# Optimization experiments

Measured on AMD Instinct MI355X. Metric: run time of the kernel, lower is better.

The kernel has to match this reference:

```python
import jax, jax.numpy as jnp
import numpy as np

N = 4096
FIN = 4096
LOC = 16
H1, H2, HEADS = 120, 50, 4
H1_PER = H1 // HEADS
FILM_Z = 32
SSDB_H = 60
N_HEMI = N // 2
NEG_SLOPE = 0.1
GATE_BIAS = -2.0
MASK_FILL = -9e15


def leaky(x):
    return jax.nn.leaky_relu(x, negative_slope=NEG_SLOPE)


def gat(x, mask, W, a_src, a_dst, bias, concat):
    # x: (N, Fin), W: (H, Fin, O), a_src/a_dst: (H, O), mask: (N, N) bool
    wh = jnp.einsum('nf,hfo->hno', x, W)            # (H, N, O)
    f1 = jnp.einsum('hno,ho->hn', wh, a_src)        # (H, N)
    f2 = jnp.einsum('hno,ho->hn', wh, a_dst)        # (H, N)
    e = leaky(f1[:, :, None] + f2[:, None, :])      # (H, N, N)
    e = jnp.where(mask[None], e, MASK_FILL)
    alpha = jax.nn.softmax(e, axis=-1)
    out = jnp.einsum('hij,hjo->hio', alpha, wh)     # (H, N, O)
    if concat:
        h, n, o = out.shape
        out2 = out.transpose(1, 0, 2).reshape(n, h * o)
    else:
        out2 = out.mean(axis=0)
    return out2 + bias


def _uni(k, shape, stdv):
    return jax.random.uniform(k, shape, jnp.float32, -stdv, stdv)


def setup_inputs() -> dict:
    key = jax.random.key(0)
    ks = jax.random.split(key, 30)
    s1 = 1.0 / np.sqrt(H1_PER)
    s2 = 1.0 / np.sqrt(H2)
    inp = {
        'x_fc': jax.random.normal(ks[0], (N, FIN), jnp.float32),
        'adj': jax.random.randint(ks[1], (N, N), 0, 2, jnp.int32),
        'l_loc': jax.random.uniform(ks[2], (N, LOC), jnp.float32),
        # gat1
        'W1': _uni(ks[3], (HEADS, FIN, H1_PER), s1),
        'a1s': _uni(ks[4], (HEADS, H1_PER), s1),
        'a1d': _uni(ks[5], (HEADS, H1_PER), s1),
        'b1': _uni(ks[6], (H1,), s1),
        # gat2
        'W2': _uni(ks[7], (1, H1, H2), s2),
        'a2s': _uni(ks[8], (1, H2), s2),
        'a2d': _uni(ks[9], (1, H2), s2),
        'b2': _uni(ks[10], (H2,), s2),
        # classifier (no bias)
        'Wc': _uni(ks[11], (2, H2), s2),
        # FiLM trunk
        'Wl1': _uni(ks[12], (FILM_Z, LOC), 1.0 / np.sqrt(LOC)),
        'bl1': _uni(ks[13], (FILM_Z,), 1.0 / np.sqrt(LOC)),
        'Wl2': _uni(ks[14], (FILM_Z, FILM_Z), 1.0 / np.sqrt(FILM_Z)),
        'bl2': _uni(ks[15], (FILM_Z,), 1.0 / np.sqrt(FILM_Z)),
        'Wg': _uni(ks[16], (H2, FILM_Z), 1.0 / np.sqrt(FILM_Z)),
        'bg': _uni(ks[17], (H2,), 1.0 / np.sqrt(FILM_Z)),
        'Wb': _uni(ks[18], (H2, FILM_Z), 1.0 / np.sqrt(FILM_Z)),
        'bb': _uni(ks[19], (H2,), 1.0 / np.sqrt(FILM_Z)),
        'Wgate': _uni(ks[20], (1, FILM_Z), 1.0 / np.sqrt(FILM_Z)),
        'bgate': jnp.full((1,), GATE_BIAS, jnp.float32),
        # SSDB hemi
        'Ws1': _uni(ks[21], (SSDB_H, N_HEMI), 1.0 / np.sqrt(N_HEMI)),
        'bs1': _uni(ks[22], (SSDB_H,), 1.0 / np.sqrt(N_HEMI)),
        'Ws2': _uni(ks[23], (1, SSDB_H), 1.0 / np.sqrt(SSDB_H)),
        'bs2': _uni(ks[24], (1,), 1.0 / np.sqrt(SSDB_H)),
    }
    return inp


def reference(x_fc, adj, l_loc, W1, a1s, a1d, b1, W2, a2s, a2d, b2, Wc,
              Wl1, bl1, Wl2, bl2, Wg, bg, Wb, bb, Wgate, bgate,
              Ws1, bs1, Ws2, bs2):
    mask = adj > 0
    h = leaky(gat(x_fc, mask, W1, a1s, a1d, b1, concat=True))    # (N, 120)
    h = leaky(gat(h, mask, W2, a2s, a2d, b2, concat=False))      # (N, 50)
    # FiLM conditioning
    z = leaky(l_loc @ Wl1.T + bl1)
    z = leaky(z @ Wl2.T + bl2)
    gamma = z @ Wg.T + bg                                        # (N, 50)
    beta = z @ Wb.T + bb                                         # (N, 50)
    g = jax.nn.sigmoid(z @ Wgate.T + bgate)                      # (N, 1)
    cov = jnp.clip(l_loc[:, -1], 0.0, 1.0)                       # coverage_power = 1.0
    g = g * cov[:, None]
    h_fused = h + g * (gamma * h + beta)
    logits = leaky(h_fused @ Wc.T)                               # (N, 2)
    # hemisphere SSDB bias
    t = logits.T                                                 # (2, N)
    ipsi = t[:, :N_HEMI]
    contra = t[:, N_HEMI:2 * N_HEMI]
    h_i = leaky(ipsi @ Ws1.T + bs1)                              # (2, 60)
    h_c = leaky(contra @ Ws1.T + bs1)
    b_i = leaky(h_i @ Ws2.T + bs2)                               # (2, 1)
    b_c = leaky(h_c @ Ws2.T + bs2)
    b_mid = 0.5 * (b_i + b_c)                                    # (2, 1)
    bias_nodes = jnp.concatenate([
        jnp.broadcast_to(b_i.T, (N_HEMI, 2)),
        jnp.broadcast_to(b_c.T, (N_HEMI, 2)),
    ], axis=0)                                                   # n_mid = 0
    logits = logits + bias_nodes
    bias_avg = b_mid[:, 0]                                       # (2,)
    return logits, bias_avg
```

## Files before the change

kernel.cpp:

```cpp
#include <hip/hip_runtime.h>

#define NN 4096
#define NNP 4128
#define BROW 132
#define HEADS 4
#define H1PER 30
#define H1DIM 120
#define H2DIM 50

typedef short short8_t __attribute__((ext_vector_type(8)));
typedef float f32x4 __attribute__((ext_vector_type(4)));

__device__ __forceinline__ float lrelu(float x) { return x > 0.f ? x : 0.1f * x; }

__device__ __forceinline__ unsigned short bfrne(float x) {
  unsigned u = __float_as_uint(x);
  u += 0x7fffu + ((u >> 16) & 1u);
  return (unsigned short)(u >> 16);
}
__device__ __forceinline__ unsigned bfpk_rne(float lo, float hi) {
  return (unsigned)bfrne(lo) | ((unsigned)bfrne(hi) << 16);
}
__device__ __forceinline__ unsigned bfpk(float lo, float hi) {
  unsigned a = (__float_as_uint(lo) + 0x8000u) >> 16;
  unsigned b = (__float_as_uint(hi) + 0x8000u) & 0xffff0000u;
  return a | b;
}
__device__ __forceinline__ unsigned fenc(float x) {
  unsigned u = __float_as_uint(x);
  return (u & 0x80000000u) ? ~u : (u | 0x80000000u);
}
__device__ __forceinline__ float fdec(unsigned u) {
  return (u & 0x80000000u) ? __uint_as_float(u ^ 0x80000000u) : __uint_as_float(~u);
}

#define GL16(g, l)                                                                        \
  __builtin_amdgcn_global_load_lds((const __attribute__((address_space(1))) unsigned int*)(g), \
                                   (__attribute__((address_space(3))) unsigned int*)(l), 16, 0, 0)

__global__ __launch_bounds__(256) void k_bits(const int* __restrict__ adj,
                                              unsigned long long* __restrict__ bits,
                                              const float* __restrict__ W1,
                                              const float* __restrict__ a1s,
                                              const float* __restrict__ a1d,
                                              unsigned short* __restrict__ w1t,
                                              unsigned* __restrict__ mxu) {
  int t = threadIdx.x;
  if (blockIdx.x >= 16384) {
    if (blockIdx.x == 16384 && t < 8) mxu[t] = 0;
    int k = (blockIdx.x - 16384) * 256 + t;
#pragma unroll
    for (int h = 0; h < 4; ++h) {
      const float* wp = W1 + ((size_t)h * 4096 + k) * H1PER;
      float fs = 0.f, fd = 0.f;
#pragma unroll
      for (int oo = 0; oo < H1PER; ++oo) {
        float v = wp[oo];
        w1t[(size_t)(h * 30 + oo) * NNP + k] = bfrne(v);
        fs += v * a1s[h * H1PER + oo];
        fd += v * a1d[h * H1PER + oo];
      }
      w1t[(size_t)(120 + h) * NNP + k] = bfrne(fs);
      w1t[(size_t)(124 + h) * NNP + k] = bfrne(fd);
    }
    return;
  }
  int n = blockIdx.x >> 2, r = blockIdx.x & 3;
  size_t base = (size_t)n * 4096 + r * 1024;
  int v0 = adj[base + t];
  int v1 = adj[base + 256 + t];
  int v2 = adj[base + 512 + t];
  int v3 = adj[base + 768 + t];
  unsigned long long m0 = __ballot(v0 > 0);
  unsigned long long m1 = __ballot(v1 > 0);
  unsigned long long m2 = __ballot(v2 > 0);
  unsigned long long m3 = __ballot(v3 > 0);
  if ((t & 63) == 0) {
    size_t w = (size_t)n * (BROW / 2) + r * 16 + (t >> 6);
    bits[w] = m0;
    bits[w + 4] = m1;
    bits[w + 8] = m2;
    bits[w + 12] = m3;
  }
}

__global__ __launch_bounds__(256) void k_gemm1s(const float* __restrict__ x,
                                                const unsigned short* __restrict__ w1t,
                                                float* __restrict__ part) {
  const int t = threadIdx.x;
  const int lane = t & 63, wave = t >> 6;
  const int m = lane & 15, q = lane >> 4;
  const int i0 = blockIdx.x * 128;
  const int kz = blockIdx.y * 512;
  __shared__ float xs[128 * 64];
  __shared__ unsigned short bs[128 * 64];
  const int ar_ = t >> 4, ac_ = t & 15;
  const float* gxa = x + (size_t)(i0 + ar_) * 4096 + kz + (ac_ ^ (ar_ & 7)) * 4;
  const int l8 = lane >> 3, c8 = lane & 7;
  const unsigned short* gb = w1t + (size_t)(wave * 32 + l8) * NNP + kz + (c8 ^ l8) * 8;
  const int bo = wave * 2048 + lane * 8;
  const int asw = m & 7;
  f32x4 acc[2][8];
#pragma unroll
  for (int rg = 0; rg < 2; ++rg)
#pragma unroll
    for (int nt = 0; nt < 8; ++nt) acc[rg][nt] = (f32x4){0.f, 0.f, 0.f, 0.f};

#pragma unroll
  for (int it = 0; it < 8; ++it) {
    const int kc = it * 64;
#pragma unroll
    for (int i = 0; i < 8; ++i)
      GL16(gxa + (size_t)i * 16 * 4096 + kc, &xs[(i * 16 + ar_) * 64 + ac_ * 4]);
#pragma unroll
    for (int i = 0; i < 4; ++i)
      GL16(gb + (size_t)i * 8 * NNP + kc, &bs[bo + i * 512]);
    asm volatile("s_waitcnt vmcnt(0)" ::: "memory");
    __builtin_amdgcn_s_barrier();
    __builtin_amdgcn_sched_barrier(0);
#pragma unroll
    for (int ks2 = 0; ks2 < 2; ++ks2) {
      const int c0 = ks2 * 8 + q * 2;
      union { short8_t v; unsigned u[4]; } A[2];
#pragma unroll
      for (int rg = 0; rg < 2; ++rg) {
        const int arow = wave * 32 + rg * 16 + m;
        float4 a0 = *(const float4*)&xs[arow * 64 + ((c0 ^ asw) * 4)];
        float4 a1 = *(const float4*)&xs[arow * 64 + (((c0 + 1) ^ asw) * 4)];
        A[rg].u[0] = bfpk_rne(a0.x, a0.y);
        A[rg].u[1] = bfpk_rne(a0.z, a0.w);
        A[rg].u[2] = bfpk_rne(a1.x, a1.y);
        A[rg].u[3] = bfpk_rne(a1.z, a1.w);
      }
      const int bch = ((ks2 << 2) | q) ^ asw;
#pragma unroll
      for (int nt = 0; nt < 8; ++nt) {
        short8_t B = *(const short8_t*)&bs[(nt * 16 + m) * 64 + bch * 8];
        acc[0][nt] = __builtin_amdgcn_mfma_f32_16x16x32_bf16(A[0].v, B, acc[0][nt], 0, 0, 0);
        acc[1][nt] = __builtin_amdgcn_mfma_f32_16x16x32_bf16(A[1].v, B, acc[1][nt], 0, 0, 0);
      }
    }
    __builtin_amdgcn_sched_barrier(0);
    __builtin_amdgcn_s_barrier();
  }
  float* pp = part + ((size_t)blockIdx.y * 4096 + i0 + wave * 32 + q * 4) * 128 + m;
#pragma unroll
  for (int rg = 0; rg < 2; ++rg)
#pragma unroll
    for (int nt = 0; nt < 8; ++nt)
#pragma unroll
      for (int r = 0; r < 4; ++r) pp[(rg * 16 + r) * 128 + nt * 16] = acc[rg][nt][r];
}

__global__ __launch_bounds__(256) void k_f1c(const float* __restrict__ part,
                                             unsigned short* __restrict__ whbt,
                                             float* __restrict__ f1, float* __restrict__ f2,
                                             unsigned* __restrict__ mxu1) {
  const int t = threadIdx.x;
  const int n = blockIdx.x * 16 + (t >> 4);
  const int og = (t & 15) * 8;
  __shared__ float f2loc[16][4];
  float s[8] = {0.f, 0.f, 0.f, 0.f, 0.f, 0.f, 0.f, 0.f};
  for (int z = 0; z < 8; ++z) {
    const float* pp = part + ((size_t)z * NN + n) * 128 + og;
    float4 u0 = *(const float4*)pp;
    float4 u1 = *(const float4*)(pp + 4);
    s[0] += u0.x; s[1] += u0.y; s[2] += u0.z; s[3] += u0.w;
    s[4] += u1.x; s[5] += u1.y; s[6] += u1.z; s[7] += u1.w;
  }
  if (og < 120) {
#pragma unroll
    for (int j = 0; j < 8; ++j) {
      int o = og + j;
      int h = o / 30, oo = o - h * 30;
      whbt[(size_t)(h * 32 + oo) * NNP + n] = bfrne(s[j]);
    }
  } else {
#pragma unroll
    for (int j = 0; j < 4; ++j) {
      f1[(size_t)j * NN + n] = s[j];
      f2[(size_t)j * NN + n] = s[4 + j];
      f2loc[t >> 4][j] = s[4 + j];
    }
  }
  if ((t & 15) < 8) {
    int h = (t & 15) >> 1, odd = (t & 15) & 1;
    whbt[(size_t)(h * 32 + 30 + odd) * NNP + n] = odd ? 0 : 0x3f80;
  }
  __syncthreads();
  if (t < 4) {
    float m = f2loc[0][t];
#pragma unroll
    for (int i = 1; i < 16; ++i) m = fmaxf(m, f2loc[i][t]);
    atomicMax(&mxu1[t], fenc(m));
  }
}

__global__ __launch_bounds__(256) void k_att1m(const unsigned short* __restrict__ whbt,
                                               const float* __restrict__ f1, const float* __restrict__ f2,
                                               const unsigned* __restrict__ mxu1,
                                               const unsigned int* __restrict__ bits32,
                                               float* __restrict__ part) {
  const int h = blockIdx.y, js = blockIdx.z;
  const int t = threadIdx.x;
  const int lane = t & 63, wave = t >> 6;
  const int m = lane & 15, q = lane >> 4;
  const int i0w = blockIdx.x * 128 + wave * 32;
  const int jbase = js * 1024;
  const float mxh = fdec(mxu1[h]);
  __shared__ float2 es[1024];
  __shared__ unsigned short bsm1[2][8192];
  for (int e = t; e < 1024; e += 256) {
    float fv = f2[h * NN + jbase + e] - mxh;
    es[e] = make_float2(__expf(fv), __expf(0.1f * fv));
  }
  float Rr[2];
  const uint4* br[2];
#pragma unroll
  for (int rg = 0; rg < 2; ++rg) {
    const float f1r = f1[h * NN + i0w + rg * 16 + m];
    const float s = f1r + mxh;
    Rr[rg] = __expf(fminf(60.f, -0.9f * s));
    br[rg] = (const uint4*)(bits32 + (size_t)(i0w + rg * 16 + m) * BROW + (jbase >> 5));
  }
  const float2* fp = es;
  const int r_st = t >> 3;
  const unsigned short* gB = whbt + (size_t)(h * 32 + r_st) * NNP + jbase + ((t & 7) ^ (r_st & 7)) * 8;
  f32x4 acc[2][2];
#pragma unroll
  for (int rg = 0; rg < 2; ++rg) {
    acc[rg][0] = (f32x4){0.f, 0.f, 0.f, 0.f};
    acc[rg][1] = (f32x4){0.f, 0.f, 0.f, 0.f};
  }

  __syncthreads();

#pragma unroll
  for (int c = 0; c < 4; ++c) GL16(gB + c * 64, &bsm1[0][c * 2048 + t * 8]);

#pragma unroll
  for (int jc = 0; jc < 4; ++jc) {
    const int cur = jc & 1;
    uint4 bqq[2][2];
#pragma unroll
    for (int rg = 0; rg < 2; ++rg) {
      bqq[rg][0] = br[rg][jc * 2];
      bqq[rg][1] = br[rg][jc * 2 + 1];
    }
    if (jc < 3) {
#pragma unroll
      for (int c = 0; c < 4; ++c) GL16(gB + (jc + 1) * 256 + c * 64, &bsm1[cur ^ 1][c * 2048 + t * 8]);
      asm volatile("s_waitcnt vmcnt(4)" ::: "memory");
    } else {
      asm volatile("s_waitcnt vmcnt(0)" ::: "memory");
    }
    __builtin_amdgcn_s_barrier();
    __builtin_amdgcn_sched_barrier(0);
#pragma unroll
    for (int g = 0; g < 2; ++g) {
#pragma unroll
      for (int sub = 0; sub < 4; ++sub) {
        const int jl = (jc * 2 + g) * 128 + sub * 32;
        float4 e01 = *(const float4*)(fp + jl + q * 8);
        float4 e23 = *(const float4*)(fp + jl + q * 8 + 2);
        float4 e45 = *(const float4*)(fp + jl + q * 8 + 4);
        float4 e67 = *(const float4*)(fp + jl + q * 8 + 6);
        const int p = g * 16 + sub * 4 + q;
        short8_t b0 = *(const short8_t*)&bsm1[cur][(p >> 3) * 2048 + m * 64 + ((p & 7) ^ (m & 7)) * 8];
        short8_t b1 = *(const short8_t*)&bsm1[cur][(p >> 3) * 2048 + (m + 16) * 64 + ((p & 7) ^ ((m + 16) & 7)) * 8];
#pragma unroll
        for (int rg = 0; rg < 2; ++rg) {
          const uint4 bq = bqq[rg][g];
          unsigned bsel = (sub == 0 ? bq.x : sub == 1 ? bq.y : sub == 2 ? bq.z : bq.w) >> (q * 8);
          const float R = Rr[rg];
          auto sc = [&](float ep, float en, int jj) {
            float wv = fmaxf(ep, R * en);
            return ((bsel >> jj) & 1u) ? wv : 0.f;
          };
          union { short8_t v; unsigned u[4]; } A;
          A.u[0] = bfpk(sc(e01.x, e01.y, 0), sc(e01.z, e01.w, 1));
          A.u[1] = bfpk(sc(e23.x, e23.y, 2), sc(e23.z, e23.w, 3));
          A.u[2] = bfpk(sc(e45.x, e45.y, 4), sc(e45.z, e45.w, 5));
          A.u[3] = bfpk(sc(e67.x, e67.y, 6), sc(e67.z, e67.w, 7));
          acc[rg][0] = __builtin_amdgcn_mfma_f32_16x16x32_bf16(A.v, b0, acc[rg][0], 0, 0, 0);
          acc[rg][1] = __builtin_amdgcn_mfma_f32_16x16x32_bf16(A.v, b1, acc[rg][1], 0, 0, 0);
        }
      }
    }
    __builtin_amdgcn_sched_barrier(0);
    __builtin_amdgcn_s_barrier();
  }
#pragma unroll
  for (int rg = 0; rg < 2; ++rg) {
    float* pp = part + ((size_t)(js * 4 + h) * NN + i0w + rg * 16 + q * 4) * 32 + m;
#pragma unroll
    for (int r = 0; r < 4; ++r) {
      pp[r * 32] = acc[rg][0][r];
      pp[r * 32 + 16] = acc[rg][1][r];
    }
  }
}

__global__ __launch_bounds__(256) void k_fuseA(const float* __restrict__ part, const float* __restrict__ b1,
                                               const float* __restrict__ W2, const float* __restrict__ a2s,
                                               const float* __restrict__ a2d,
                                               unsigned short* __restrict__ whbt2,
                                               float* __restrict__ f1b, float* __restrict__ f2b,
                                               unsigned* __restrict__ mxu2) {
  const int t = threadIdx.x;
  __shared__ float W2s[H1DIM * H2DIM];
  __shared__ float h1s[4][124];
  __shared__ float f2red[4];
  for (int e = t; e < H1DIM * H2DIM; e += 256) W2s[e] = W2[e];
  const int wv = t >> 6, lane = t & 63;
  const int n = blockIdx.x * 4 + wv;
  const int h = lane >> 4, o2 = (lane & 15) * 2;
  float tot0 = 0.f, tot1 = 0.f;
#pragma unroll
  for (int z = 0; z < 4; ++z) {
    const float* pp = part + ((size_t)(z * 4 + h) * NN + n) * 32 + o2;
    float2 u = *(const float2*)pp;
    tot0 += u.x;
    tot1 += u.y;
  }
  float l = __shfl(tot0, h * 16 + 15);
  float inv = 1.f / l;
  if (o2 < 30) {
    h1s[wv][h * 30 + o2] = lrelu(tot0 * inv + b1[h * 30 + o2]);
    h1s[wv][h * 30 + o2 + 1] = lrelu(tot1 * inv + b1[h * 30 + o2 + 1]);
  }
  __syncthreads();
  const int o = lane;
  float acc = 0.f;
  if (o < H2DIM) {
    const float* hr = h1s[wv];
#pragma unroll 4
    for (int k = 0; k < H1DIM; ++k) acc += hr[k] * W2s[k * H2DIM + o];
  }
  unsigned short wbv = (o < H2DIM) ? bfrne(acc) : (o == H2DIM ? (unsigned short)0x3f80 : (unsigned short)0);
  whbt2[(size_t)o * NNP + n] = wbv;
  float ps = (o < H2DIM) ? acc * a2s[o] : 0.f;
  float pd = (o < H2DIM) ? acc * a2d[o] : 0.f;
  for (int off = 32; off > 0; off >>= 1) {
    ps += __shfl_down(ps, off);
    pd += __shfl_down(pd, off);
  }
  if (lane == 0) {
    f1b[n] = ps;
    f2b[n] = pd;
    f2red[wv] = pd;
  }
  __syncthreads();
  if (t == 0) {
    float m = fmaxf(fmaxf(f2red[0], f2red[1]), fmaxf(f2red[2], f2red[3]));
    atomicMax(mxu2, fenc(m));
  }
}

__global__ __launch_bounds__(256) void k_att2m(const unsigned short* __restrict__ whbt2,
                                               const float* __restrict__ f1b, const float* __restrict__ f2b,
                                               const unsigned* __restrict__ mxu2,
                                               const unsigned int* __restrict__ bits32,
                                               float* __restrict__ part) {
  const int js = blockIdx.y;
  const int t = threadIdx.x;
  const int lane = t & 63, wave = t >> 6;
  const int m = lane & 15, q = lane >> 4;
  const int i0w = blockIdx.x * 128 + wave * 32;
  const int jbase = js * 512;
  const float mx0 = fdec(mxu2[0]);
  __shared__ float2 es[512];
  __shared__ unsigned short bsm2[2][8192];
  for (int e = t; e < 512; e += 256) {
    float fv = f2b[jbase + e] - mx0;
    es[e] = make_float2(__expf(fv), __expf(0.1f * fv));
  }
  float Rr[2];
  const uint4* br[2];
#pragma unroll
  for (int rg = 0; rg < 2; ++rg) {
    const float f1r = f1b[i0w + rg * 16 + m];
    const float s = f1r + mx0;
    Rr[rg] = __expf(fminf(60.f, -0.9f * s));
    br[rg] = (const uint4*)(bits32 + (size_t)(i0w + rg * 16 + m) * BROW + (jbase >> 5));
  }
  const float2* fp = es;
  const int r2 = t >> 2;
  const int sw2 = (r2 & 3) ^ ((r2 >> 2) & 3);
  const unsigned short* gB2 = whbt2 + (size_t)r2 * NNP + jbase + ((t & 3) ^ sw2) * 8;
  f32x4 acc[2][4];
#pragma unroll
  for (int rg = 0; rg < 2; ++rg)
#pragma unroll
    for (int xx = 0; xx < 4; ++xx) acc[rg][xx] = (f32x4){0.f, 0.f, 0.f, 0.f};

  __syncthreads();

#pragma unroll
  for (int c = 0; c < 4; ++c) GL16(gB2 + c * 32, &bsm2[0][c * 2048 + t * 8]);

#pragma unroll
  for (int jc = 0; jc < 4; ++jc) {
    const int cur = jc & 1;
    uint4 bqr[2];
    bqr[0] = br[0][jc];
    bqr[1] = br[1][jc];
    if (jc < 3) {
#pragma unroll
      for (int c = 0; c < 4; ++c) GL16(gB2 + (jc + 1) * 128 + c * 32, &bsm2[cur ^ 1][c * 2048 + t * 8]);
      asm volatile("s_waitcnt vmcnt(4)" ::: "memory");
    } else {
      asm volatile("s_waitcnt vmcnt(0)" ::: "memory");
    }
    __builtin_amdgcn_s_barrier();
    __builtin_amdgcn_sched_barrier(0);
#pragma unroll
    for (int sub = 0; sub < 4; ++sub) {
      const int jl = jc * 128 + sub * 32;
      float4 e01 = *(const float4*)(fp + jl + q * 8);
      float4 e23 = *(const float4*)(fp + jl + q * 8 + 2);
      float4 e45 = *(const float4*)(fp + jl + q * 8 + 4);
      float4 e67 = *(const float4*)(fp + jl + q * 8 + 6);
      const int p = sub * 4 + q;
#pragma unroll
      for (int rg = 0; rg < 2; ++rg) {
        const uint4 bq = bqr[rg];
        unsigned bsel = (sub == 0 ? bq.x : sub == 1 ? bq.y : sub == 2 ? bq.z : bq.w) >> (q * 8);
        const float R = Rr[rg];
        auto sc = [&](float ep, float en, int jj) {
          float wv = fmaxf(ep, R * en);
          return ((bsel >> jj) & 1u) ? wv : 0.f;
        };
        union { short8_t v; unsigned u[4]; } A;
        A.u[0] = bfpk(sc(e01.x, e01.y, 0), sc(e01.z, e01.w, 1));
        A.u[1] = bfpk(sc(e23.x, e23.y, 2), sc(e23.z, e23.w, 3));
        A.u[2] = bfpk(sc(e45.x, e45.y, 4), sc(e45.z, e45.w, 5));
        A.u[3] = bfpk(sc(e67.x, e67.y, 6), sc(e67.z, e67.w, 7));
#pragma unroll
        for (int tile = 0; tile < 4; ++tile) {
          const int f = tile * 16 + m;
          const int sw = (f & 3) ^ ((f >> 2) & 3);
          short8_t b = *(const short8_t*)&bsm2[cur][(p >> 2) * 2048 + f * 32 + (((p & 3) ^ sw)) * 8];
          acc[rg][tile] = __builtin_amdgcn_mfma_f32_16x16x32_bf16(A.v, b, acc[rg][tile], 0, 0, 0);
        }
      }
    }
    __builtin_amdgcn_sched_barrier(0);
    __builtin_amdgcn_s_barrier();
  }
#pragma unroll
  for (int rg = 0; rg < 2; ++rg) {
    float* pp = part + ((size_t)js * NN + i0w + rg * 16 + q * 4) * 64 + m;
#pragma unroll
    for (int tile = 0; tile < 4; ++tile)
#pragma unroll
      for (int r = 0; r < 4; ++r) pp[r * 64 + tile * 16] = acc[rg][tile][r];
  }
}

__global__ __launch_bounds__(256) void k_fuseB(const float* __restrict__ part, const float* __restrict__ b2,
                                               const float* __restrict__ l_loc,
                                               const float* __restrict__ Wl1, const float* __restrict__ bl1,
                                               const float* __restrict__ Wl2, const float* __restrict__ bl2,
                                               const float* __restrict__ Wg, const float* __restrict__ bg,
                                               const float* __restrict__ Wb, const float* __restrict__ bb,
                                               const float* __restrict__ Wgate, const float* __restrict__ bgate,
                                               const float* __restrict__ Wc, float* __restrict__ logits) {
  const int t = threadIdx.x;
  const int wv = t >> 6, lane = t & 63;
  const int n = blockIdx.x * 4 + wv;
  const float* p = part + (size_t)n * 64 + lane;
  float tot = 0.f;
#pragma unroll
  for (int z = 0; z < 8; ++z) tot += p[(size_t)z * NN * 64];
  float l = __shfl(tot, 50);
  float hv = (lane < H2DIM) ? lrelu(tot / l + b2[lane]) : 0.f;
  int r32 = lane & 31;
  float locv = l_loc[n * 16 + (lane & 15)];
  float cov = __shfl(locv, 15);
  cov = fminf(fmaxf(cov, 0.f), 1.f);
  float a1v = bl1[r32];
#pragma unroll
  for (int j = 0; j < 16; ++j) a1v += Wl1[r32 * 16 + j] * __shfl(locv, j);
  float z1 = lrelu(a1v);
  float a2v = bl2[r32];
#pragma unroll
  for (int j = 0; j < 32; ++j) a2v += Wl2[r32 * 32 + j] * __shfl(z1, j);
  float z2 = lrelu(a2v);
  float gs = bgate[0];
  float gam, bet;
  {
    int o = lane < H2DIM ? lane : 0;
    gam = bg[o];
    bet = bb[o];
#pragma unroll
    for (int j = 0; j < 32; ++j) {
      float zj = __shfl(z2, j);
      gs += Wgate[j] * zj;
      gam += Wg[o * 32 + j] * zj;
      bet += Wb[o * 32 + j] * zj;
    }
  }
  float g = cov / (1.f + __expf(-gs));
  float hf = hv + g * (gam * hv + bet);
  int o = lane < H2DIM ? lane : 0;
  float p0 = lane < H2DIM ? hf * Wc[o] : 0.f;
  float p1 = lane < H2DIM ? hf * Wc[H2DIM + o] : 0.f;
  for (int off = 32; off > 0; off >>= 1) {
    p0 += __shfl_down(p0, off);
    p1 += __shfl_down(p1, off);
  }
  if (lane == 0) {
    logits[n * 2 + 0] = lrelu(p0);
    logits[n * 2 + 1] = lrelu(p1);
  }
}

__global__ __launch_bounds__(64) void k_ssdbA(const float* __restrict__ logits,
                                              const float* __restrict__ Ws1, const float* __restrict__ bs1,
                                              const float* __restrict__ Ws2, float* __restrict__ hsum) {
  const int k = blockIdx.x, combo = blockIdx.y;
  const int hemi = combo >> 1, c = combo & 1;
  const int lane = threadIdx.x;
  const float* wr = Ws1 + (size_t)k * 2048;
  const float* lc = logits + (size_t)hemi * 4096 + c;
  float acc = 0.f;
#pragma unroll 4
  for (int i = lane; i < 2048; i += 64) acc += wr[i] * lc[2 * i];
  for (int off = 32; off > 0; off >>= 1) acc += __shfl_down(acc, off);
  if (lane == 0) hsum[combo * 60 + k] = lrelu(acc + bs1[k]) * Ws2[k];
}

__global__ __launch_bounds__(256) void k_finB(const float* __restrict__ hsum,
                                              const float* __restrict__ bs2,
                                              const float* __restrict__ logits,
                                              float* __restrict__ out) {
  __shared__ float Bs[4];
  const int t = threadIdx.x;
  {
    int combo = t >> 6, k = t & 63;
    float v = (k < 60) ? hsum[combo * 60 + k] : 0.f;
    for (int off = 32; off > 0; off >>= 1) v += __shfl_down(v, off);
    if (k == 0) Bs[combo] = lrelu(v + bs2[0]);
  }
  __syncthreads();
  int id = blockIdx.x * 256 + t;
  if (id < 2 * NN) {
    int n = id >> 1, c = id & 1;
    out[id] = logits[id] + Bs[(n < 2048 ? 0 : 2) + c];
  } else if (id < 2 * NN + 2) {
    int c = id - 2 * NN;
    out[id] = 0.5f * (Bs[c] + Bs[2 + c]);
  }
}

#define OFF_BITS 0
#define OFF_W1T 540672
#define OFF_GP 804864
#define OFF_A1P 804864
#define OFF_A2P 804864
#define OFF_WH1BT 4999168
#define OFF_F1A 5263360
#define OFF_F2A 5279744
#define OFF_WH2BT 5296128
#define OFF_F12 5428224
#define OFF_F22 5432320
#define OFF_LOG 5436416
#define OFF_MX 5444608
#define OFF_HS 5444672

extern "C" void kernel_launch(void* const* d_in, const int* in_sizes, int n_in,
                              void* d_out, int out_size, void* d_ws, size_t ws_size,
                              hipStream_t stream) {
  const float* x_fc  = (const float*)d_in[0];
  const int*   adj   = (const int*)d_in[1];
  const float* l_loc = (const float*)d_in[2];
  const float* W1    = (const float*)d_in[3];
  const float* a1s   = (const float*)d_in[4];
  const float* a1d   = (const float*)d_in[5];
  const float* b1    = (const float*)d_in[6];
  const float* W2    = (const float*)d_in[7];
  const float* a2s   = (const float*)d_in[8];
  const float* a2d   = (const float*)d_in[9];
  const float* b2    = (const float*)d_in[10];
  const float* Wc    = (const float*)d_in[11];
  const float* Wl1   = (const float*)d_in[12];
  const float* bl1   = (const float*)d_in[13];
  const float* Wl2   = (const float*)d_in[14];
  const float* bl2   = (const float*)d_in[15];
  const float* Wg    = (const float*)d_in[16];
  const float* bg    = (const float*)d_in[17];
  const float* Wb    = (const float*)d_in[18];
  const float* bb    = (const float*)d_in[19];
  const float* Wgate = (const float*)d_in[20];
  const float* bgate = (const float*)d_in[21];
  const float* Ws1   = (const float*)d_in[22];
  const float* bs1   = (const float*)d_in[23];
  const float* Ws2   = (const float*)d_in[24];
  const float* bs2   = (const float*)d_in[25];
  float* out = (float*)d_out;
  float* w = (float*)d_ws;
  unsigned long long* bits = (unsigned long long*)(w + OFF_BITS);
  const unsigned int* bits32 = (const unsigned int*)bits;
  unsigned short* wh1bt = (unsigned short*)(w + OFF_WH1BT);
  unsigned short* wh2bt = (unsigned short*)(w + OFF_WH2BT);
  unsigned short* w1t = (unsigned short*)(w + OFF_W1T);
  unsigned* mxu = (unsigned*)(w + OFF_MX);

  k_bits<<<16400, 256, 0, stream>>>(adj, bits, W1, a1s, a1d, w1t, mxu);
  k_gemm1s<<<dim3(32, 8), 256, 0, stream>>>(x_fc, w1t, w + OFF_GP);
  k_f1c<<<256, 256, 0, stream>>>(w + OFF_GP, wh1bt, w + OFF_F1A, w + OFF_F2A, mxu);
  k_att1m<<<dim3(32, HEADS, 4), 256, 0, stream>>>(wh1bt, w + OFF_F1A, w + OFF_F2A,
                                                  mxu, bits32, w + OFF_A1P);
  k_fuseA<<<1024, 256, 0, stream>>>(w + OFF_A1P, b1, W2, a2s, a2d, wh2bt,
                                    w + OFF_F12, w + OFF_F22, mxu + 4);
  k_att2m<<<dim3(32, 8), 256, 0, stream>>>(wh2bt, w + OFF_F12, w + OFF_F22,
                                           mxu + 4, bits32, w + OFF_A2P);
  k_fuseB<<<1024, 256, 0, stream>>>(w + OFF_A2P, b2, l_loc, Wl1, bl1, Wl2, bl2,
                                    Wg, bg, Wb, bb, Wgate, bgate, Wc, w + OFF_LOG);
  k_ssdbA<<<dim3(60, 4), 64, 0, stream>>>(w + OFF_LOG, Ws1, bs1, Ws2, w + OFF_HS);
  k_finB<<<33, 256, 0, stream>>>(w + OFF_HS, bs2, w + OFF_LOG, out);
}
```

Before: 303.1 us.

## Double-buffer LDS staging in gemm1 split-K kernel with smaller K tile

Replaces the single-buffered 64-wide K tile in k_gemm1s with two 32-wide LDS buffers. The next tile's global-to-LDS loads are issued before computing on the current one, with a partial vmcnt wait. The intent is to overlap memory latency with the MFMA work instead of stalling on a full wait every iteration. In exchange there are twice as many iterations and barriers, and a new XOR swizzle for the B tile that must avoid bank conflicts.

```diff
diff --git a/kernel.cpp b/kernel.cpp
--- a/kernel.cpp
+++ b/kernel.cpp
@@ -92,13 +92,13 @@
   const int m = lane & 15, q = lane >> 4;
   const int i0 = blockIdx.x * 128;
   const int kz = blockIdx.y * 512;
-  __shared__ float xs[128 * 64];
-  __shared__ unsigned short bs[128 * 64];
-  const int ar_ = t >> 4, ac_ = t & 15;
-  const float* gxa = x + (size_t)(i0 + ar_) * 4096 + kz + (ac_ ^ (ar_ & 7)) * 4;
-  const int l8 = lane >> 3, c8 = lane & 7;
-  const unsigned short* gb = w1t + (size_t)(wave * 32 + l8) * NNP + kz + (c8 ^ l8) * 8;
-  const int bo = wave * 2048 + lane * 8;
+  __shared__ float xs[2][128 * 32];
+  __shared__ unsigned short bs[2][128 * 32];
+  const int ar_ = t >> 3, ac_ = t & 7;
+  const float* gxa = x + (size_t)(i0 + ar_) * 4096 + kz + ((ac_ ^ (ar_ & 7)) * 4);
+  const int br_ = t >> 2;
+  const int bsw = (br_ & 3) ^ ((br_ >> 2) & 3);
+  const unsigned short* gwb = w1t + (size_t)br_ * NNP + kz + ((t & 3) ^ bsw) * 8;
   const int asw = m & 7;
   f32x4 acc[2][8];
 #pragma unroll
@@ -106,39 +106,46 @@
 #pragma unroll
     for (int nt = 0; nt < 8; ++nt) acc[rg][nt] = (f32x4){0.f, 0.f, 0.f, 0.f};
 
-#pragma unroll
-  for (int it = 0; it < 8; ++it) {
-    const int kc = it * 64;
-#pragma unroll
-    for (int i = 0; i < 8; ++i)
-      GL16(gxa + (size_t)i * 16 * 4096 + kc, &xs[(i * 16 + ar_) * 64 + ac_ * 4]);
+  auto STAGE = [&](int buf, int kk) {
 #pragma unroll
     for (int i = 0; i < 4; ++i)
-      GL16(gb + (size_t)i * 8 * NNP + kc, &bs[bo + i * 512]);
-    asm volatile("s_waitcnt vmcnt(0)" ::: "memory");
+      GL16(gxa + (size_t)i * 32 * 4096 + kk, &xs[buf][(i * 32 + ar_) * 32 + ac_ * 4]);
+#pragma unroll
+    for (int i = 0; i < 2; ++i)
+      GL16(gwb + (size_t)i * 64 * NNP + kk, &bs[buf][(i * 64 + br_) * 32 + (t & 3) * 8]);
+  };
+
+  STAGE(0, 0);
+#pragma unroll
+  for (int it = 0; it < 16; ++it) {
+    const int cur = it & 1;
+    if (it < 15) {
+      STAGE(cur ^ 1, (it + 1) * 32);
+      asm volatile("s_waitcnt vmcnt(6)" ::: "memory");
+    } else {
+      asm volatile("s_waitcnt vmcnt(0)" ::: "memory");
+    }
     __builtin_amdgcn_s_barrier();
     __builtin_amdgcn_sched_barrier(0);
-#pragma unroll
-    for (int ks2 = 0; ks2 < 2; ++ks2) {
-      const int c0 = ks2 * 8 + q * 2;
-      union { short8_t v; unsigned u[4]; } A[2];
-#pragma unroll
-      for (int rg = 0; rg < 2; ++rg) {
-        const int arow = wave * 32 + rg * 16 + m;
-        float4 a0 = *(const float4*)&xs[arow * 64 + ((c0 ^ asw) * 4)];
-        float4 a1 = *(const float4*)&xs[arow * 64 + (((c0 + 1) ^ asw) * 4)];
-        A[rg].u[0] = bfpk_rne(a0.x, a0.y);
-        A[rg].u[1] = bfpk_rne(a0.z, a0.w);
-        A[rg].u[2] = bfpk_rne(a1.x, a1.y);
-        A[rg].u[3] = bfpk_rne(a1.z, a1.w);
-      }
-      const int bch = ((ks2 << 2) | q) ^ asw;
-#pragma unroll
-      for (int nt = 0; nt < 8; ++nt) {
-        short8_t B = *(const short8_t*)&bs[(nt * 16 + m) * 64 + bch * 8];
-        acc[0][nt] = __builtin_amdgcn_mfma_f32_16x16x32_bf16(A[0].v, B, acc[0][nt], 0, 0, 0);
-        acc[1][nt] = __builtin_amdgcn_mfma_f32_16x16x32_bf16(A[1].v, B, acc[1][nt], 0, 0, 0);
-      }
+    const int c0 = q * 2;
+    union { short8_t v; unsigned u[4]; } A[2];
+#pragma unroll
+    for (int rg = 0; rg < 2; ++rg) {
+      const int arow = wave * 32 + rg * 16 + m;
+      float4 a0 = *(const float4*)&xs[cur][arow * 32 + ((c0 ^ asw) * 4)];
+      float4 a1 = *(const float4*)&xs[cur][arow * 32 + (((c0 + 1) ^ asw) * 4)];
+      A[rg].u[0] = bfpk_rne(a0.x, a0.y);
+      A[rg].u[1] = bfpk_rne(a0.z, a0.w);
+      A[rg].u[2] = bfpk_rne(a1.x, a1.y);
+      A[rg].u[3] = bfpk_rne(a1.z, a1.w);
+    }
+#pragma unroll
+    for (int nt = 0; nt < 8; ++nt) {
+      const int f = nt * 16 + m;
+      const int fsw = (f & 3) ^ ((f >> 2) & 3);
+      short8_t B = *(const short8_t*)&bs[cur][f * 32 + ((q ^ fsw) * 8)];
+      acc[0][nt] = __builtin_amdgcn_mfma_f32_16x16x32_bf16(A[0].v, B, acc[0][nt], 0, 0, 0);
+      acc[1][nt] = __builtin_amdgcn_mfma_f32_16x16x32_bf16(A[1].v, B, acc[1][nt], 0, 0, 0);
     }
     __builtin_amdgcn_sched_barrier(0);
     __builtin_amdgcn_s_barrier();
```

New measurement: 300.1 us. Within noise of the previous version (-1.0%).
